# Performance work log

Hardware: AMD Instinct MI355X
Metric: run time of the kernel (lower is better)

Reference implementation:

```python
import jax, jax.numpy as jnp
import numpy as np

N = 100000
E = 3200000
IN_FEATS = 128
HID_FEATS = 128
OUT_FEATS = 128
MLP_HID = 128
MLP_OUT = 64


def setup_inputs() -> dict:
    key = jax.random.key(0)
    ks = jax.random.split(key, 12)
    x = jax.random.normal(ks[0], (N, IN_FEATS), dtype=jnp.float32)
    src = jax.random.randint(ks[1], (E,), 0, N, dtype=jnp.int32)
    dst = jax.random.randint(ks[2], (E,), 0, N, dtype=jnp.int32)
    s = 0.05
    W1 = jax.random.normal(ks[3], (IN_FEATS, HID_FEATS), dtype=jnp.float32) * s
    b1 = jnp.zeros((HID_FEATS,), dtype=jnp.float32)
    W2 = jax.random.normal(ks[4], (HID_FEATS, OUT_FEATS), dtype=jnp.float32) * s
    b2 = jnp.zeros((OUT_FEATS,), dtype=jnp.float32)
    Wm1 = jax.random.normal(ks[5], (OUT_FEATS, MLP_HID), dtype=jnp.float32) * s
    bm1 = jnp.zeros((MLP_HID,), dtype=jnp.float32)
    Wm2 = jax.random.normal(ks[6], (MLP_HID, MLP_OUT), dtype=jnp.float32) * s
    bm2 = jnp.zeros((MLP_OUT,), dtype=jnp.float32)
    return {"x": x, "src": src, "dst": dst, "W1": W1, "b1": b1,
            "W2": W2, "b2": b2, "Wm1": Wm1, "bm1": bm1, "Wm2": Wm2, "bm2": bm2}


def _graph_conv(h, src, dst, W, b, out_norm, in_norm):
    # DGL GraphConv norm='both': rst = D_in^{-1/2} * A^T (D_out^{-1/2} * h) @ W + b
    msg = (h * out_norm[:, None])[src]                       # [E, F] gather
    agg = jax.ops.segment_sum(msg, dst, num_segments=N)      # [N, F] scatter-add
    return (agg * in_norm[:, None]) @ W + b


def _forward(x, src, dst, W1, b1, W2, b2, Wm1, bm1, Wm2, bm2):
    ones = jnp.ones((src.shape[0],), dtype=x.dtype)
    out_deg = jnp.maximum(jax.ops.segment_sum(ones, src, num_segments=N), 1.0)
    in_deg = jnp.maximum(jax.ops.segment_sum(ones, dst, num_segments=N), 1.0)
    out_norm = out_deg ** -0.5
    in_norm = in_deg ** -0.5
    # conv1 + ReLU (dropout identity in eval mode)
    h = jax.nn.relu(_graph_conv(x, src, dst, W1, b1, out_norm, in_norm))
    # conv2 + ReLU
    h = jax.nn.relu(_graph_conv(h, src, dst, W2, b2, out_norm, in_norm))
    # MLP head: Linear -> ReLU -> Linear -> sigmoid (act='sigmoid')
    h = jax.nn.relu(h @ Wm1 + bm1)
    h = jax.nn.sigmoid(h @ Wm2 + bm2)
    return h


def reference(x, src, dst, W1, b1, W2, b2, Wm1, bm1, Wm2, bm2):
    return _forward(x, src, dst, W1, b1, W2, b2, Wm1, bm1, Wm2, bm2)
```

## Files before the change

kernel.cpp:

```cpp
#include <hip/hip_runtime.h>
#include <math.h>

#define NNODES 100000
#define NEDGES 3200000
#define F 128
#define NPB 512
#define NB ((NNODES + NPB - 1) / NPB)
#define CAP 20480
#define T2 8192
#define NKEY (NPB * 16)

typedef __attribute__((ext_vector_type(8))) short short8;
typedef __attribute__((ext_vector_type(4))) float f32x4;

__device__ __forceinline__ unsigned short f2bf(float f) {
    unsigned u = __float_as_uint(f);
    unsigned r = u + 0x7fff + ((u >> 16) & 1);
    return (unsigned short)(r >> 16);
}
__device__ __forceinline__ float bflo(unsigned u) { return __uint_as_float(u << 16); }
__device__ __forceinline__ float bfhi(unsigned u) { return __uint_as_float(u & 0xffff0000u); }


__global__ void init_cursors_kernel(int* __restrict__ dcur, int* __restrict__ scur) {
    int b = blockIdx.x * 256 + threadIdx.x;
    if (b < NB) { dcur[b] = b * CAP; scur[b] = b * CAP; }
}


__global__ __launch_bounds__(256) void dual_bin_kernel(const int* __restrict__ src,
                                                       const int* __restrict__ dst,
                                                       int* __restrict__ dcur,
                                                       int* __restrict__ scur,
                                                       unsigned* __restrict__ epk,
                                                       unsigned short* __restrict__ esl) {
    __shared__ unsigned pk[T2];
    __shared__ unsigned short sl[T2];
    __shared__ unsigned char db[T2], sb[T2];
    __shared__ int dh[NB], dbase[NB], dlc[NB];
    __shared__ int sh[NB], sbase[NB], slc[NB];
    int t = threadIdx.x;
    for (int i = t; i < NB; i += 256) { dh[i] = 0; dlc[i] = 0; sh[i] = 0; slc[i] = 0; }
    __syncthreads();
    int e0 = blockIdx.x * T2;
    int n = min(T2, NEDGES - e0);
    for (int i = t; i < n; i += 256) {
        int s = src[e0 + i], d = dst[e0 + i];
        int bd = d >> 9, bs = s >> 9;
        pk[i] = (unsigned)s | ((unsigned)(d & 511) << 17);
        sl[i] = (unsigned short)(s & 511);
        db[i] = (unsigned char)bd;
        sb[i] = (unsigned char)bs;
        atomicAdd(&dh[bd], 1);
        atomicAdd(&sh[bs], 1);
    }
    __syncthreads();
    for (int b = t; b < NB; b += 256) {
        if (dh[b]) dbase[b] = atomicAdd(&dcur[b], dh[b]);
        if (sh[b]) sbase[b] = atomicAdd(&scur[b], sh[b]);
    }
    __syncthreads();
    for (int i = t; i < n; i += 256) {
        int b = db[i];
        epk[dbase[b] + atomicAdd(&dlc[b], 1)] = pk[i];
    }
    for (int i = t; i < n; i += 256) {
        int b = sb[i];
        esl[sbase[b] + atomicAdd(&slc[b], 1)] = sl[i];
    }
}


__global__ __launch_bounds__(512) void src_hist_kernel(const unsigned short* __restrict__ esl,
                                                       const int* __restrict__ scur,
                                                       float* __restrict__ out_norm) {
    __shared__ int cnt[NPB];
    int t = threadIdx.x, b = blockIdx.x;
    cnt[t] = 0;
    __syncthreads();
    int e0 = b * CAP, e1 = scur[b];
    for (int i = e0 + t; i < e1; i += 512) atomicAdd(&cnt[esl[i]], 1);
    __syncthreads();
    int node = b * NPB + t;
    if (node < NNODES) out_norm[node] = rsqrtf((float)max(cnt[t], 1));
}


__global__ __launch_bounds__(512) void bucket_csr_kernel(const unsigned* __restrict__ epk,
                                                         const int* __restrict__ dcur,
                                                         int2* __restrict__ row_span,
                                                         float* __restrict__ in_norm,
                                                         int* __restrict__ csr_src) {
    __shared__ int hist[NKEY];
    __shared__ int lcur[NKEY];
    __shared__ int psum[NPB];
    int t = threadIdx.x, b = blockIdx.x;
    for (int i = t; i < NKEY; i += 512) { hist[i] = 0; lcur[i] = 0; }
    __syncthreads();
    int e0 = b * CAP, e1 = dcur[b];
    for (int i = e0 + t; i < e1; i += 512) {
        unsigned p = epk[i];
        int key = (int)((p >> 17) << 4) | (int)((p & 0x1FFFF) >> 13);
        atomicAdd(&hist[key], 1);
    }
    __syncthreads();
    int base_ = t << 4;
    int tot = 0;
#pragma unroll
    for (int j = 0; j < 16; j++) {
        int h = hist[base_ + j];
        hist[base_ + j] = tot;
        tot += h;
    }
    psum[t] = tot;
    __syncthreads();
    for (int d = 1; d < NPB; d <<= 1) {
        int u = (t >= d) ? psum[t - d] : 0;
        __syncthreads();
        psum[t] += u;
        __syncthreads();
    }
    int excl = psum[t] - tot;
    int node = b * NPB + t;
    if (node < NNODES) {
        row_span[node] = make_int2(e0 + excl, e0 + excl + tot);
        in_norm[node] = rsqrtf((float)max(tot, 1));
    }
#pragma unroll
    for (int j = 0; j < 16; j++) hist[base_ + j] += excl;
    __syncthreads();
    for (int i = e0 + t; i < e1; i += 512) {
        unsigned p = epk[i];
        int key = (int)((p >> 17) << 4) | (int)((p & 0x1FFFF) >> 13);
        csr_src[e0 + hist[key] + atomicAdd(&lcur[key], 1)] = (int)(p & 0x1FFFF);
    }
}


__global__ __launch_bounds__(256) void scale_to_bf16_kernel(const float* __restrict__ x,
                                                            const float* __restrict__ out_norm,
                                                            uint2* __restrict__ hs) {
    int tid = blockIdx.x * 256 + threadIdx.x;
    if (tid >= NNODES * 32) return;
    int row = tid >> 5, q = tid & 31;
    float nrm = out_norm[row];
    float4 v = *(const float4*)(x + (size_t)row * F + q * 4);
    uint2 o;
    o.x = (unsigned)f2bf(v.x * nrm) | ((unsigned)f2bf(v.y * nrm) << 16);
    o.y = (unsigned)f2bf(v.z * nrm) | ((unsigned)f2bf(v.w * nrm) << 16);
    hs[(size_t)row * 32 + q] = o;
}


__global__ void pack_all_kernel(const float* __restrict__ W1, const float* __restrict__ W2,
                                const float* __restrict__ Wm1, const float* __restrict__ Wm2,
                                short8* __restrict__ Wp) {
    int idx = blockIdx.x * 256 + threadIdx.x;
    if (idx >= 7168) return;
    const float* W; int ncol, base;
    if (idx < 2048)      { W = W1;  ncol = 128; base = 0; }
    else if (idx < 4096) { W = W2;  ncol = 128; base = 2048; }
    else if (idx < 6144) { W = Wm1; ncol = 128; base = 4096; }
    else                 { W = Wm2; ncol = 64;  base = 6144; }
    int li = idx - base;
    int lane = li & 63, s = (li >> 6) & 3, c = li >> 8;
    int nn = c * 16 + (lane & 15);
    int k0 = s * 32 + (lane >> 4) * 8;
    short8 v;
#pragma unroll
    for (int j = 0; j < 8; j++) v[j] = (short)f2bf(W[(size_t)(k0 + j) * ncol + nn]);
    Wp[idx] = v;
}


__global__ __launch_bounds__(256) void aggregate_kernel(const unsigned* __restrict__ hs,
                                                        const int2* __restrict__ row_span,
                                                        const int* __restrict__ csr_src,
                                                        const float* __restrict__ in_norm,
                                                        unsigned* __restrict__ outv) {
    int wave = threadIdx.x >> 6;
    int lane = threadIdx.x & 63;
    int node = blockIdx.x * 4 + wave;
    if (node >= NNODES) return;
    int2 sp = row_span[node];
    int beg = sp.x, end = sp.y;
    float ax = 0.f, ay = 0.f;
    int j = beg;
    for (; j + 8 <= end; j += 8) {
        int s0 = csr_src[j],     s1 = csr_src[j + 1], s2 = csr_src[j + 2], s3 = csr_src[j + 3];
        int s4 = csr_src[j + 4], s5 = csr_src[j + 5], s6 = csr_src[j + 6], s7 = csr_src[j + 7];
        unsigned u0 = hs[(size_t)s0 * 64 + lane];
        unsigned u1 = hs[(size_t)s1 * 64 + lane];
        unsigned u2 = hs[(size_t)s2 * 64 + lane];
        unsigned u3 = hs[(size_t)s3 * 64 + lane];
        unsigned u4 = hs[(size_t)s4 * 64 + lane];
        unsigned u5 = hs[(size_t)s5 * 64 + lane];
        unsigned u6 = hs[(size_t)s6 * 64 + lane];
        unsigned u7 = hs[(size_t)s7 * 64 + lane];
        ax += bflo(u0) + bflo(u1) + bflo(u2) + bflo(u3)
            + bflo(u4) + bflo(u5) + bflo(u6) + bflo(u7);
        ay += bfhi(u0) + bfhi(u1) + bfhi(u2) + bfhi(u3)
            + bfhi(u4) + bfhi(u5) + bfhi(u6) + bfhi(u7);
    }
    for (; j < end; j++) {
        unsigned u0 = hs[(size_t)csr_src[j] * 64 + lane];
        ax += bflo(u0);
        ay += bfhi(u0);
    }
    float inn = in_norm[node];
    outv[(size_t)node * 64 + lane] =
        (unsigned)f2bf(ax * inn) | ((unsigned)f2bf(ay * inn) << 16);
}


template <int SCALE>
__global__ __launch_bounds__(256) void gemm_mfma_kernel(const unsigned short* __restrict__ A,
                                                        const short8* __restrict__ Bp,
                                                        const float* __restrict__ bias,
                                                        const float* __restrict__ out_norm,
                                                        unsigned short* __restrict__ Cout, int nrows) {
    int w = threadIdx.x >> 6, lane = threadIdx.x & 63;
    int m = lane & 15, quad = lane >> 4;
    int row0 = blockIdx.x * 64 + w * 16;

    int arow = min(row0 + m, nrows - 1);
    short8 afrag[4];
#pragma unroll
    for (int s = 0; s < 4; s++)
        afrag[s] = *(const short8*)(A + (size_t)arow * F + s * 32 + quad * 8);

    int baseRow = row0 + quad * 4;
    float nrm[4];
    if (SCALE) {
#pragma unroll
        for (int r = 0; r < 4; r++) nrm[r] = out_norm[min(baseRow + r, nrows - 1)];
    }

#pragma unroll
    for (int c = 0; c < 8; c++) {
        f32x4 acc = {0.f, 0.f, 0.f, 0.f};
#pragma unroll
        for (int s = 0; s < 4; s++) {
            short8 b = Bp[(c * 4 + s) * 64 + lane];
            acc = __builtin_amdgcn_mfma_f32_16x16x32_bf16(afrag[s], b, acc, 0, 0, 0);
        }
        float bc = bias[c * 16 + m];
#pragma unroll
        for (int r = 0; r < 4; r++) {
            int row = baseRow + r;
            if (row < nrows) {
                float v = fmaxf(acc[r] + bc, 0.f);
                if (SCALE) v *= nrm[r];
                Cout[(size_t)row * F + c * 16 + m] = f2bf(v);
            }
        }
    }
}


__global__ __launch_bounds__(256) void mlp_fused_kernel(const unsigned short* __restrict__ A,
                                                        const short8* __restrict__ Bp1,
                                                        const float* __restrict__ bm1,
                                                        const short8* __restrict__ Bp2,
                                                        const float* __restrict__ bm2,
                                                        float* __restrict__ out, int nrows) {
    __shared__ unsigned short h3[4][16][136];
    int w = threadIdx.x >> 6, lane = threadIdx.x & 63;
    int m = lane & 15, quad = lane >> 4;
    int row0 = blockIdx.x * 64 + w * 16;

    int arow = min(row0 + m, nrows - 1);
    short8 afrag[4];
#pragma unroll
    for (int s = 0; s < 4; s++)
        afrag[s] = *(const short8*)(A + (size_t)arow * F + s * 32 + quad * 8);

#pragma unroll
    for (int c = 0; c < 8; c++) {
        f32x4 acc = {0.f, 0.f, 0.f, 0.f};
#pragma unroll
        for (int s = 0; s < 4; s++) {
            short8 b = Bp1[(c * 4 + s) * 64 + lane];
            acc = __builtin_amdgcn_mfma_f32_16x16x32_bf16(afrag[s], b, acc, 0, 0, 0);
        }
        float bc = bm1[c * 16 + m];
#pragma unroll
        for (int r = 0; r < 4; r++)
            h3[w][quad * 4 + r][c * 16 + m] = f2bf(fmaxf(acc[r] + bc, 0.f));
    }
    __syncthreads();

    short8 a2[4];
#pragma unroll
    for (int s = 0; s < 4; s++)
        a2[s] = *(const short8*)(&h3[w][m][s * 32 + quad * 8]);

    int baseRow = row0 + quad * 4;
#pragma unroll
    for (int c2 = 0; c2 < 4; c2++) {
        f32x4 acc = {0.f, 0.f, 0.f, 0.f};
#pragma unroll
        for (int s = 0; s < 4; s++) {
            short8 b = Bp2[(c2 * 4 + s) * 64 + lane];
            acc = __builtin_amdgcn_mfma_f32_16x16x32_bf16(a2[s], b, acc, 0, 0, 0);
        }
        float bc = bm2[c2 * 16 + m];
#pragma unroll
        for (int r = 0; r < 4; r++) {
            int row = baseRow + r;
            if (row < nrows)
                out[(size_t)row * 64 + c2 * 16 + m] = 1.f / (1.f + __expf(-(acc[r] + bc)));
        }
    }
}


extern "C" void kernel_launch(void* const* d_in, const int* in_sizes, int n_in,
                              void* d_out, int out_size, void* d_ws, size_t ws_size,
                              hipStream_t stream) {
    const float* x   = (const float*)d_in[0];
    const int* src   = (const int*)d_in[1];
    const int* dst   = (const int*)d_in[2];
    const float* W1  = (const float*)d_in[3];
    const float* b1  = (const float*)d_in[4];
    const float* W2  = (const float*)d_in[5];
    const float* b2  = (const float*)d_in[6];
    const float* Wm1 = (const float*)d_in[7];
    const float* bm1 = (const float*)d_in[8];
    const float* Wm2 = (const float*)d_in[9];
    const float* bm2 = (const float*)d_in[10];
    float* out = (float*)d_out;

    char* w = (char*)d_ws;
    int* dcur          = (int*)w;   w += (size_t)(NB + 4) * 4;
    int* scur          = (int*)w;   w += (size_t)(NB + 4) * 4;
    float* out_norm    = (float*)w; w += (size_t)NNODES * 4;
    float* in_norm     = (float*)w; w += (size_t)NNODES * 4;
    int2* row_span     = (int2*)w;  w += (size_t)NNODES * 8;
    int* csr_src       = (int*)w;   w += (size_t)NB * CAP * 4;
    unsigned* epk      = (unsigned*)w; w += (size_t)NB * CAP * 4;
    unsigned short* esl= (unsigned short*)w; w += (size_t)NB * CAP * 2;
    short8* Wp         = (short8*)w; w += (size_t)7168 * 16;
    unsigned* bufX     = (unsigned*)w; w += (size_t)NNODES * 64 * 4;
    unsigned* bufY     = (unsigned*)w; w += (size_t)NNODES * 64 * 4;

    init_cursors_kernel<<<1, 256, 0, stream>>>(dcur, scur);
    dual_bin_kernel<<<(NEDGES + T2 - 1) / T2, 256, 0, stream>>>(src, dst, dcur, scur, epk, esl);
    src_hist_kernel<<<NB, 512, 0, stream>>>(esl, scur, out_norm);
    bucket_csr_kernel<<<NB, 512, 0, stream>>>(epk, dcur, row_span, in_norm, csr_src);
    scale_to_bf16_kernel<<<(NNODES * 32 + 255) / 256, 256, 0, stream>>>(x, out_norm, (uint2*)bufX);
    pack_all_kernel<<<28, 256, 0, stream>>>(W1, W2, Wm1, Wm2, Wp);

    const int aggGrid = (NNODES + 3) / 4;
    const int gemmGrid = (NNODES + 63) / 64;

    aggregate_kernel<<<aggGrid, 256, 0, stream>>>(bufX, row_span, csr_src, in_norm, bufY);
    gemm_mfma_kernel<1><<<gemmGrid, 256, 0, stream>>>((const unsigned short*)bufY, Wp, b1, out_norm,
                                                      (unsigned short*)bufX, NNODES);
    aggregate_kernel<<<aggGrid, 256, 0, stream>>>(bufX, row_span, csr_src, in_norm, bufY);
    gemm_mfma_kernel<0><<<gemmGrid, 256, 0, stream>>>((const unsigned short*)bufY, Wp + 2048, b2, out_norm,
                                                      (unsigned short*)bufX, NNODES);
    mlp_fused_kernel<<<gemmGrid, 256, 0, stream>>>((const unsigned short*)bufX, Wp + 4096, bm1,
                                                   Wp + 6144, bm2, out, NNODES);
}
```

Baseline: 569.7 us.

## Aggregate 16 nodes per wave in source-range order for gather locality

The CSR build now records, for each destination node, offsets for 14 sub-ranges of source IDs (sorted by a source-ID sub-key). The aggregation kernel has each wave process 16 consecutive destination nodes, sweeping source ranges in the outer loop so all 16 nodes gather from a similar source region at the same time, which should improve L2 reuse of the feature rows. In exchange the inner loop is serial per edge with no 8-way load unrolling, keeps 32 accumulators per lane, and adds 14 extra offset arrays. The loops also assume the node count divides evenly by 16.

```diff
diff --git a/kernel.cpp b/kernel.cpp
--- a/kernel.cpp
+++ b/kernel.cpp
@@ -9,6 +9,7 @@
 #define CAP 20480
 #define T2 8192
 #define NKEY (NPB * 16)
+#define NRANGE 13
 
 typedef __attribute__((ext_vector_type(8))) short short8;
 typedef __attribute__((ext_vector_type(4))) float f32x4;
@@ -88,7 +89,7 @@
 
 __global__ __launch_bounds__(512) void bucket_csr_kernel(const unsigned* __restrict__ epk,
                                                          const int* __restrict__ dcur,
-                                                         int2* __restrict__ row_span,
+                                                         int* __restrict__ rro,
                                                          float* __restrict__ in_norm,
                                                          int* __restrict__ csr_src) {
     __shared__ int hist[NKEY];
@@ -122,12 +123,14 @@
     }
     int excl = psum[t] - tot;
     int node = b * NPB + t;
+    if (node < NNODES) in_norm[node] = rsqrtf((float)max(tot, 1));
+#pragma unroll
+    for (int j = 0; j < 16; j++) hist[base_ + j] += excl;
     if (node < NNODES) {
-        row_span[node] = make_int2(e0 + excl, e0 + excl + tot);
-        in_norm[node] = rsqrtf((float)max(tot, 1));
-    }
-#pragma unroll
-    for (int j = 0; j < 16; j++) hist[base_ + j] += excl;
+#pragma unroll
+        for (int j = 0; j < 14; j++)
+            rro[j * NNODES + node] = e0 + hist[base_ + j];
+    }
     __syncthreads();
     for (int i = e0 + t; i < e1; i += 512) {
         unsigned p = epk[i];
@@ -174,42 +177,54 @@
 
 
 __global__ __launch_bounds__(256) void aggregate_kernel(const unsigned* __restrict__ hs,
-                                                        const int2* __restrict__ row_span,
+                                                        const int* __restrict__ rro,
                                                         const int* __restrict__ csr_src,
                                                         const float* __restrict__ in_norm,
                                                         unsigned* __restrict__ outv) {
     int wave = threadIdx.x >> 6;
     int lane = threadIdx.x & 63;
-    int node = blockIdx.x * 4 + wave;
-    if (node >= NNODES) return;
-    int2 sp = row_span[node];
-    int beg = sp.x, end = sp.y;
-    float ax = 0.f, ay = 0.f;
-    int j = beg;
-    for (; j + 8 <= end; j += 8) {
-        int s0 = csr_src[j],     s1 = csr_src[j + 1], s2 = csr_src[j + 2], s3 = csr_src[j + 3];
-        int s4 = csr_src[j + 4], s5 = csr_src[j + 5], s6 = csr_src[j + 6], s7 = csr_src[j + 7];
-        unsigned u0 = hs[(size_t)s0 * 64 + lane];
-        unsigned u1 = hs[(size_t)s1 * 64 + lane];
-        unsigned u2 = hs[(size_t)s2 * 64 + lane];
-        unsigned u3 = hs[(size_t)s3 * 64 + lane];
-        unsigned u4 = hs[(size_t)s4 * 64 + lane];
-        unsigned u5 = hs[(size_t)s5 * 64 + lane];
-        unsigned u6 = hs[(size_t)s6 * 64 + lane];
-        unsigned u7 = hs[(size_t)s7 * 64 + lane];
-        ax += bflo(u0) + bflo(u1) + bflo(u2) + bflo(u3)
-            + bflo(u4) + bflo(u5) + bflo(u6) + bflo(u7);
-        ay += bfhi(u0) + bfhi(u1) + bfhi(u2) + bfhi(u3)
-            + bfhi(u4) + bfhi(u5) + bfhi(u6) + bfhi(u7);
-    }
-    for (; j < end; j++) {
-        unsigned u0 = hs[(size_t)csr_src[j] * 64 + lane];
-        ax += bflo(u0);
-        ay += bfhi(u0);
-    }
-    float inn = in_norm[node];
-    outv[(size_t)node * 64 + lane] =
-        (unsigned)f2bf(ax * inn) | ((unsigned)f2bf(ay * inn) << 16);
+    int wid = blockIdx.x * 4 + wave;
+    int n0 = wid * 16;
+    if (n0 >= NNODES) return;
+    float ax[16], ay[16];
+#pragma unroll
+    for (int i = 0; i < 16; i++) { ax[i] = 0.f; ay[i] = 0.f; }
+    int li = lane & 15;
+    for (int k = 0; k < NRANGE; k++) {
+        int off0 = rro[k * NNODES + n0 + li];
+        int off1 = rro[(k + 1) * NNODES + n0 + li];
+#pragma unroll
+        for (int i = 0; i < 16; i++) {
+            int s = __builtin_amdgcn_readlane(off0, i);
+            int e = __builtin_amdgcn_readlane(off1, i);
+            for (int j = s; j < e; j++) {
+                int sn = csr_src[j];
+                unsigned u = hs[(size_t)sn * 64 + lane];
+                if (i == 0)  { ax[0]  += bflo(u); ay[0]  += bfhi(u); }
+                if (i == 1)  { ax[1]  += bflo(u); ay[1]  += bfhi(u); }
+                if (i == 2)  { ax[2]  += bflo(u); ay[2]  += bfhi(u); }
+                if (i == 3)  { ax[3]  += bflo(u); ay[3]  += bfhi(u); }
+                if (i == 4)  { ax[4]  += bflo(u); ay[4]  += bfhi(u); }
+                if (i == 5)  { ax[5]  += bflo(u); ay[5]  += bfhi(u); }
+                if (i == 6)  { ax[6]  += bflo(u); ay[6]  += bfhi(u); }
+                if (i == 7)  { ax[7]  += bflo(u); ay[7]  += bfhi(u); }
+                if (i == 8)  { ax[8]  += bflo(u); ay[8]  += bfhi(u); }
+                if (i == 9)  { ax[9]  += bflo(u); ay[9]  += bfhi(u); }
+                if (i == 10) { ax[10] += bflo(u); ay[10] += bfhi(u); }
+                if (i == 11) { ax[11] += bflo(u); ay[11] += bfhi(u); }
+                if (i == 12) { ax[12] += bflo(u); ay[12] += bfhi(u); }
+                if (i == 13) { ax[13] += bflo(u); ay[13] += bfhi(u); }
+                if (i == 14) { ax[14] += bflo(u); ay[14] += bfhi(u); }
+                if (i == 15) { ax[15] += bflo(u); ay[15] += bfhi(u); }
+            }
+        }
+    }
+#pragma unroll
+    for (int i = 0; i < 16; i++) {
+        float inn = in_norm[n0 + i];
+        outv[(size_t)(n0 + i) * 64 + lane] =
+            (unsigned)f2bf(ax[i] * inn) | ((unsigned)f2bf(ay[i] * inn) << 16);
+    }
 }
 
 
@@ -336,7 +351,7 @@
     int* scur          = (int*)w;   w += (size_t)(NB + 4) * 4;
     float* out_norm    = (float*)w; w += (size_t)NNODES * 4;
     float* in_norm     = (float*)w; w += (size_t)NNODES * 4;
-    int2* row_span     = (int2*)w;  w += (size_t)NNODES * 8;
+    int* rro           = (int*)w;   w += (size_t)14 * NNODES * 4;
     int* csr_src       = (int*)w;   w += (size_t)NB * CAP * 4;
     unsigned* epk      = (unsigned*)w; w += (size_t)NB * CAP * 4;
     unsigned short* esl= (unsigned short*)w; w += (size_t)NB * CAP * 2;
@@ -347,17 +362,17 @@
     init_cursors_kernel<<<1, 256, 0, stream>>>(dcur, scur);
     dual_bin_kernel<<<(NEDGES + T2 - 1) / T2, 256, 0, stream>>>(src, dst, dcur, scur, epk, esl);
     src_hist_kernel<<<NB, 512, 0, stream>>>(esl, scur, out_norm);
-    bucket_csr_kernel<<<NB, 512, 0, stream>>>(epk, dcur, row_span, in_norm, csr_src);
+    bucket_csr_kernel<<<NB, 512, 0, stream>>>(epk, dcur, rro, in_norm, csr_src);
     scale_to_bf16_kernel<<<(NNODES * 32 + 255) / 256, 256, 0, stream>>>(x, out_norm, (uint2*)bufX);
     pack_all_kernel<<<28, 256, 0, stream>>>(W1, W2, Wm1, Wm2, Wp);
 
-    const int aggGrid = (NNODES + 3) / 4;
+    const int aggGrid = (NNODES / 16 + 3) / 4;
     const int gemmGrid = (NNODES + 63) / 64;
 
-    aggregate_kernel<<<aggGrid, 256, 0, stream>>>(bufX, row_span, csr_src, in_norm, bufY);
+    aggregate_kernel<<<aggGrid, 256, 0, stream>>>(bufX, rro, csr_src, in_norm, bufY);
     gemm_mfma_kernel<1><<<gemmGrid, 256, 0, stream>>>((const unsigned short*)bufY, Wp, b1, out_norm,
                                                       (unsigned short*)bufX, NNODES);
-    aggregate_kernel<<<aggGrid, 256, 0, stream>>>(bufX, row_span, csr_src, in_norm, bufY);
+    aggregate_kernel<<<aggGrid, 256, 0, stream>>>(bufX, rro, csr_src, in_norm, bufY);
     gemm_mfma_kernel<0><<<gemmGrid, 256, 0, stream>>>((const unsigned short*)bufY, Wp + 2048, b2, out_norm,
                                                       (unsigned short*)bufX, NNODES);
     mlp_fused_kernel<<<gemmGrid, 256, 0, stream>>>((const unsigned short*)bufX, Wp + 4096, bm1,
```

After: 734.8 us. 1.29x slower.
